# Kernel optimization log

Hardware: AMD Instinct MI355X
Metric: run time of the kernel (lower is better)

## Reference

```python
import jax, jax.numpy as jnp
import numpy as np

MEM_DIM = 2048
BATCH = 4096


def setup_inputs() -> dict:
    key = jax.random.key(0)
    ks = jax.random.split(key, 8)
    D = MEM_DIM
    scale = 1.0 / np.sqrt(D)  # torch nn.Linear default init range ~ U(-1/sqrt(D), 1/sqrt(D))
    lc = jax.random.normal(ks[0], (BATCH, D), dtype=jnp.float32)
    lh = jax.random.normal(ks[1], (BATCH, D), dtype=jnp.float32)
    rc = jax.random.normal(ks[2], (BATCH, D), dtype=jnp.float32)
    rh = jax.random.normal(ks[3], (BATCH, D), dtype=jnp.float32)
    # Fused params: columns [0:D]=input gate, [D:2D]=left forget, [2D:3D]=right forget, [3D:4D]=update
    Wl = jax.random.uniform(ks[4], (D, 4 * D), dtype=jnp.float32, minval=-scale, maxval=scale)
    Wr = jax.random.uniform(ks[5], (D, 4 * D), dtype=jnp.float32, minval=-scale, maxval=scale)
    bl = jax.random.uniform(ks[6], (4 * D,), dtype=jnp.float32, minval=-scale, maxval=scale)
    br = jax.random.uniform(ks[7], (4 * D,), dtype=jnp.float32, minval=-scale, maxval=scale)
    return {"lc": lc, "lh": lh, "rc": rc, "rh": rh, "Wl": Wl, "bl": bl, "Wr": Wr, "br": br}


def reference(lc, lh, rc, rh, Wl, bl, Wr, br):
    D = lh.shape[-1]
    # Two fused GEMMs replace 8 separate mem_dim x mem_dim linears (same math).
    g = jnp.dot(lh, Wl) + bl + jnp.dot(rh, Wr) + br  # [B, 4D]
    i = jax.nn.sigmoid(g[:, 0 * D:1 * D])   # input gate
    lf = jax.nn.sigmoid(g[:, 1 * D:2 * D])  # left forget gate
    rf = jax.nn.sigmoid(g[:, 2 * D:3 * D])  # right forget gate
    u = jnp.tanh(g[:, 3 * D:4 * D])         # cell update
    c = i * u + lf * lc + rf * rc
    h = jnp.tanh(c)
    return (c, h)
```

## Files before the change

kernel.cpp:

```cpp
#include <hip/hip_runtime.h>
#include <stdint.h>

#define D_MEM 2048
#define BATCH 4096
#define K_DIM 4096
#define N_DIM 8192

typedef __bf16 bf16x8 __attribute__((ext_vector_type(8)));
typedef float f32x4 __attribute__((ext_vector_type(4)));

typedef const void __attribute__((address_space(1)))* gas_t;
typedef void __attribute__((address_space(3)))* las_t;

__device__ __forceinline__ ushort f2b(float f) {
  union { float f; uint32_t u; } v; v.f = f;
  uint32_t u = v.u + 0x7fffu + ((v.u >> 16) & 1u);
  return (ushort)(u >> 16);
}
__device__ __forceinline__ float b2f(ushort s) {
  union { uint32_t u; float f; } v; v.u = ((uint32_t)s) << 16;
  return v.f;
}
__device__ __forceinline__ float sigm(float x) {
  return 1.0f / (1.0f + __expf(-x));
}

__global__ void cast_concat_kernel(const float* __restrict__ lh,
                                   const float* __restrict__ rh,
                                   ushort* __restrict__ A) {
  int i4 = blockIdx.x * 256 + threadIdx.x;
  int row = i4 >> 10;
  int col = (i4 & 1023) * 4;
  const float* src = (col < D_MEM) ? (lh + (size_t)row * D_MEM + col)
                                   : (rh + (size_t)row * D_MEM + (col - D_MEM));
  float4 v = *(const float4*)src;
  ushort4 o; o.x = f2b(v.x); o.y = f2b(v.y); o.z = f2b(v.z); o.w = f2b(v.w);
  *(ushort4*)(A + (size_t)row * K_DIM + col) = o;
}

__global__ void transpose_cast_kernel(const float* __restrict__ Wl,
                                      const float* __restrict__ Wr,
                                      ushort* __restrict__ Bt) {
  __shared__ float t[64 * 65];
  const float* W = blockIdx.z ? Wr : Wl;
  int n0 = blockIdx.x * 64;
  int k0 = blockIdx.y * 64;
  int tid = threadIdx.x;
#pragma unroll
  for (int i = 0; i < 4; ++i) {
    int idx = i * 256 + tid;
    int rr = idx >> 4;
    int c4 = (idx & 15) * 4;
    float4 v = *(const float4*)(W + (size_t)(k0 + rr) * N_DIM + n0 + c4);
    t[rr * 65 + c4 + 0] = v.x;
    t[rr * 65 + c4 + 1] = v.y;
    t[rr * 65 + c4 + 2] = v.z;
    t[rr * 65 + c4 + 3] = v.w;
  }
  __syncthreads();
  int kbase = (blockIdx.z ? D_MEM : 0) + k0;
#pragma unroll
  for (int i = 0; i < 4; ++i) {
    int idx = i * 256 + tid;
    int rr = idx >> 4;
    int c4 = (idx & 15) * 4;
    ushort4 o;
    o.x = f2b(t[(c4 + 0) * 65 + rr]);
    o.y = f2b(t[(c4 + 1) * 65 + rr]);
    o.z = f2b(t[(c4 + 2) * 65 + rr]);
    o.w = f2b(t[(c4 + 3) * 65 + rr]);
    *(ushort4*)(Bt + (size_t)(n0 + rr) * K_DIM + kbase + c4) = o;
  }
}

__global__ __launch_bounds__(256) void gemm_bf16_kernel(
    const ushort* __restrict__ A,
    const ushort* __restrict__ B,
    ushort* __restrict__ C) {
  const int N = N_DIM, K = K_DIM;
  __shared__ ushort As[128 * 64];
  __shared__ ushort Bs[128 * 64];
  int tid = threadIdx.x;
  int lane = tid & 63;
  int wave = tid >> 6;
  int wm = wave >> 1, wn = wave & 1;
  int q = lane >> 4, r = lane & 15;
  int m0 = blockIdx.y * 128, n0 = blockIdx.x * 128;

  int c_chunk = (tid & 7) ^ ((tid >> 3) & 7);
  int srow = tid >> 3;
  const ushort* pA = A + (size_t)(m0 + srow) * K + c_chunk * 8;
  const ushort* pB = B + (size_t)(n0 + srow) * K + c_chunk * 8;

  int aoff[4], boff[4];
#pragma unroll
  for (int f = 0; f < 4; ++f) {
    int ml = wm * 64 + f * 16 + r;
    aoff[f] = (ml * 8 + (q ^ (ml & 7))) * 16;
    int nl = wn * 64 + f * 16 + r;
    boff[f] = (nl * 8 + (q ^ (nl & 7))) * 16;
  }

  f32x4 acc[4][4];
#pragma unroll
  for (int i = 0; i < 4; ++i)
#pragma unroll
    for (int j = 0; j < 4; ++j) acc[i][j] = f32x4{0.f, 0.f, 0.f, 0.f};

  char* AsB = (char*)As;
  char* BsB = (char*)Bs;
  int ldsbase = wave * 1024;

  for (int kt = 0; kt < K / 64; ++kt) {
#pragma unroll
    for (int t2 = 0; t2 < 4; ++t2)
      __builtin_amdgcn_global_load_lds((gas_t)(pA + (size_t)t2 * 32 * K),
                                       (las_t)(AsB + t2 * 4096 + ldsbase),
                                       16, 0, 0);
#pragma unroll
    for (int t2 = 0; t2 < 4; ++t2)
      __builtin_amdgcn_global_load_lds((gas_t)(pB + (size_t)t2 * 32 * K),
                                       (las_t)(BsB + t2 * 4096 + ldsbase),
                                       16, 0, 0);
    __syncthreads();
#pragma unroll
    for (int ks = 0; ks < 2; ++ks) {
      bf16x8 af[4], bg[4];
#pragma unroll
      for (int f = 0; f < 4; ++f) {
        af[f] = *(const bf16x8*)(AsB + (aoff[f] ^ (ks * 64)));
        bg[f] = *(const bf16x8*)(BsB + (boff[f] ^ (ks * 64)));
      }
#pragma unroll
      for (int i = 0; i < 4; ++i)
#pragma unroll
        for (int j = 0; j < 4; ++j)
          acc[i][j] = __builtin_amdgcn_mfma_f32_16x16x32_bf16(
              af[i], bg[j], acc[i][j], 0, 0, 0);
    }
    __syncthreads();
    pA += 64;
    pB += 64;
  }

#pragma unroll
  for (int i = 0; i < 4; ++i) {
    int gm_base = m0 + wm * 64 + i * 16 + q * 4;
#pragma unroll
    for (int j = 0; j < 4; ++j) {
      int gn = n0 + wn * 64 + j * 16 + r;
      size_t base = (size_t)gm_base * N + gn;
#pragma unroll
      for (int e = 0; e < 4; ++e)
        C[base + (size_t)e * N] = f2b(acc[i][j][e]);
    }
  }
}

__global__ void gate_kernel(const ushort* __restrict__ G,
                            const float* __restrict__ bl,
                            const float* __restrict__ br,
                            const float* __restrict__ lc,
                            const float* __restrict__ rc,
                            float* __restrict__ out) {
  int i4 = blockIdx.x * 256 + threadIdx.x;
  int row = i4 >> 9;
  int col = (i4 & 511) * 4;
  size_t gbase = (size_t)row * N_DIM + col;

  ushort4 ui = *(const ushort4*)(G + gbase);
  ushort4 uf = *(const ushort4*)(G + gbase + 1 * D_MEM);
  ushort4 ug = *(const ushort4*)(G + gbase + 2 * D_MEM);
  ushort4 uu = *(const ushort4*)(G + gbase + 3 * D_MEM);

  float4 bli = *(const float4*)(bl + col);
  float4 blf = *(const float4*)(bl + col + 1 * D_MEM);
  float4 blr = *(const float4*)(bl + col + 2 * D_MEM);
  float4 blu = *(const float4*)(bl + col + 3 * D_MEM);
  float4 bri = *(const float4*)(br + col);
  float4 brf = *(const float4*)(br + col + 1 * D_MEM);
  float4 brr = *(const float4*)(br + col + 2 * D_MEM);
  float4 bru = *(const float4*)(br + col + 3 * D_MEM);

  float4 vlc = *(const float4*)(lc + (size_t)row * D_MEM + col);
  float4 vrc = *(const float4*)(rc + (size_t)row * D_MEM + col);

  float4 vc, vh;
  {
    float gi = b2f(ui.x) + bli.x + bri.x;
    float gf = b2f(uf.x) + blf.x + brf.x;
    float gr = b2f(ug.x) + blr.x + brr.x;
    float gu = b2f(uu.x) + blu.x + bru.x;
    vc.x = sigm(gi) * tanhf(gu) + sigm(gf) * vlc.x + sigm(gr) * vrc.x;
    vh.x = tanhf(vc.x);
  }
  {
    float gi = b2f(ui.y) + bli.y + bri.y;
    float gf = b2f(uf.y) + blf.y + brf.y;
    float gr = b2f(ug.y) + blr.y + brr.y;
    float gu = b2f(uu.y) + blu.y + bru.y;
    vc.y = sigm(gi) * tanhf(gu) + sigm(gf) * vlc.y + sigm(gr) * vrc.y;
    vh.y = tanhf(vc.y);
  }
  {
    float gi = b2f(ui.z) + bli.z + bri.z;
    float gf = b2f(uf.z) + blf.z + brf.z;
    float gr = b2f(ug.z) + blr.z + brr.z;
    float gu = b2f(uu.z) + blu.z + bru.z;
    vc.z = sigm(gi) * tanhf(gu) + sigm(gf) * vlc.z + sigm(gr) * vrc.z;
    vh.z = tanhf(vc.z);
  }
  {
    float gi = b2f(ui.w) + bli.w + bri.w;
    float gf = b2f(uf.w) + blf.w + brf.w;
    float gr = b2f(ug.w) + blr.w + brr.w;
    float gu = b2f(uu.w) + blu.w + bru.w;
    vc.w = sigm(gi) * tanhf(gu) + sigm(gf) * vlc.w + sigm(gr) * vrc.w;
    vh.w = tanhf(vc.w);
  }

  size_t obase = (size_t)row * D_MEM + col;
  *(float4*)(out + obase) = vc;
  *(float4*)(out + (size_t)BATCH * D_MEM + obase) = vh;
}

extern "C" void kernel_launch(void* const* d_in, const int* in_sizes, int n_in,
                              void* d_out, int out_size, void* d_ws, size_t ws_size,
                              hipStream_t stream) {
  const float* lc = (const float*)d_in[0];
  const float* lh = (const float*)d_in[1];
  const float* rc = (const float*)d_in[2];
  const float* rh = (const float*)d_in[3];
  const float* Wl = (const float*)d_in[4];
  const float* bl = (const float*)d_in[5];
  const float* Wr = (const float*)d_in[6];
  const float* br = (const float*)d_in[7];
  float* out = (float*)d_out;

  char* ws = (char*)d_ws;
  ushort* A  = (ushort*)ws;
  ushort* Bt = (ushort*)(ws + (size_t)32 * 1024 * 1024);
  ushort* G  = (ushort*)(ws + (size_t)96 * 1024 * 1024);

  cast_concat_kernel<<<16384, 256, 0, stream>>>(lh, rh, A);
  dim3 tg(128, 32, 2);
  transpose_cast_kernel<<<tg, 256, 0, stream>>>(Wl, Wr, Bt);
  dim3 gg(64, 32);
  gemm_bf16_kernel<<<gg, 256, 0, stream>>>(A, Bt, G);
  gate_kernel<<<8192, 256, 0, stream>>>(G, bl, br, lc, rc, out);
}
```

Baseline: 553.3 us.

## Fuse gate epilogue into GEMM by permuting weight columns per tile

The transposed weight columns are permuted so that each 128-column GEMM tile holds all four gates for the same 32 hidden units. Each lane then has the i/f/r/u accumulators for one output element and can apply the LSTM gate math directly in the GEMM epilogue. This removes the bf16 intermediate G, its write and re-read, and the separate gate kernel launch. tanhf is also replaced with an exp-based fast tanh. The epilogue now uses scalar, strided lc/rc loads and output stores instead of float4 accesses, and it adds some accuracy risk from the approximate tanh.

```diff
diff --git a/kernel.cpp b/kernel.cpp
--- a/kernel.cpp
+++ b/kernel.cpp
@@ -17,12 +17,13 @@
   uint32_t u = v.u + 0x7fffu + ((v.u >> 16) & 1u);
   return (ushort)(u >> 16);
 }
-__device__ __forceinline__ float b2f(ushort s) {
-  union { uint32_t u; float f; } v; v.u = ((uint32_t)s) << 16;
-  return v.f;
-}
 __device__ __forceinline__ float sigm(float x) {
   return 1.0f / (1.0f + __expf(-x));
+}
+__device__ __forceinline__ float fast_tanh(float x) {
+  float xx = fminf(fmaxf(x, -15.f), 15.f);
+  float t = __expf(-2.f * xx);
+  return (1.f - t) / (1.f + t);
 }
 
 __global__ void cast_concat_kernel(const float* __restrict__ lh,
@@ -59,25 +60,33 @@
   }
   __syncthreads();
   int kbase = (blockIdx.z ? D_MEM : 0) + k0;
+  int g  = n0 >> 11;
+  int jb = n0 & 2047;
 #pragma unroll
   for (int i = 0; i < 4; ++i) {
     int idx = i * 256 + tid;
     int rr = idx >> 4;
     int c4 = (idx & 15) * 4;
+    int j = jb + rr;
+    int np = ((j >> 5) << 7) + (((j >> 4) & 1) << 6) + (g << 4) + (j & 15);
     ushort4 o;
     o.x = f2b(t[(c4 + 0) * 65 + rr]);
     o.y = f2b(t[(c4 + 1) * 65 + rr]);
     o.z = f2b(t[(c4 + 2) * 65 + rr]);
     o.w = f2b(t[(c4 + 3) * 65 + rr]);
-    *(ushort4*)(Bt + (size_t)(n0 + rr) * K_DIM + kbase + c4) = o;
-  }
-}
-
-__global__ __launch_bounds__(256) void gemm_bf16_kernel(
+    *(ushort4*)(Bt + (size_t)np * K_DIM + kbase + c4) = o;
+  }
+}
+
+__global__ __launch_bounds__(256) void gemm_gate_kernel(
     const ushort* __restrict__ A,
     const ushort* __restrict__ B,
-    ushort* __restrict__ C) {
-  const int N = N_DIM, K = K_DIM;
+    const float* __restrict__ bl,
+    const float* __restrict__ br,
+    const float* __restrict__ lc,
+    const float* __restrict__ rc,
+    float* __restrict__ out) {
+  const int K = K_DIM;
   __shared__ ushort As[128 * 64];
   __shared__ ushort Bs[128 * 64];
   int tid = threadIdx.x;
@@ -143,85 +152,28 @@
     pB += 64;
   }
 
+  int colb = (blockIdx.x << 5) + (wn << 4) + r;
+  float bsum0 = bl[0 * D_MEM + colb] + br[0 * D_MEM + colb];
+  float bsum1 = bl[1 * D_MEM + colb] + br[1 * D_MEM + colb];
+  float bsum2 = bl[2 * D_MEM + colb] + br[2 * D_MEM + colb];
+  float bsum3 = bl[3 * D_MEM + colb] + br[3 * D_MEM + colb];
+  float* outc = out;
+  float* outh = out + (size_t)BATCH * D_MEM;
 #pragma unroll
   for (int i = 0; i < 4; ++i) {
-    int gm_base = m0 + wm * 64 + i * 16 + q * 4;
-#pragma unroll
-    for (int j = 0; j < 4; ++j) {
-      int gn = n0 + wn * 64 + j * 16 + r;
-      size_t base = (size_t)gm_base * N + gn;
-#pragma unroll
-      for (int e = 0; e < 4; ++e)
-        C[base + (size_t)e * N] = f2b(acc[i][j][e]);
+    int mb = m0 + wm * 64 + i * 16 + q * 4;
+#pragma unroll
+    for (int e = 0; e < 4; ++e) {
+      size_t off = (size_t)(mb + e) * D_MEM + colb;
+      float gi = acc[i][0][e] + bsum0;
+      float gf = acc[i][1][e] + bsum1;
+      float gr = acc[i][2][e] + bsum2;
+      float gu = acc[i][3][e] + bsum3;
+      float cc = sigm(gi) * fast_tanh(gu) + sigm(gf) * lc[off] + sigm(gr) * rc[off];
+      outc[off] = cc;
+      outh[off] = fast_tanh(cc);
     }
   }
-}
-
-__global__ void gate_kernel(const ushort* __restrict__ G,
-                            const float* __restrict__ bl,
-                            const float* __restrict__ br,
-                            const float* __restrict__ lc,
-                            const float* __restrict__ rc,
-                            float* __restrict__ out) {
-  int i4 = blockIdx.x * 256 + threadIdx.x;
-  int row = i4 >> 9;
-  int col = (i4 & 511) * 4;
-  size_t gbase = (size_t)row * N_DIM + col;
-
-  ushort4 ui = *(const ushort4*)(G + gbase);
-  ushort4 uf = *(const ushort4*)(G + gbase + 1 * D_MEM);
-  ushort4 ug = *(const ushort4*)(G + gbase + 2 * D_MEM);
-  ushort4 uu = *(const ushort4*)(G + gbase + 3 * D_MEM);
-
-  float4 bli = *(const float4*)(bl + col);
-  float4 blf = *(const float4*)(bl + col + 1 * D_MEM);
-  float4 blr = *(const float4*)(bl + col + 2 * D_MEM);
-  float4 blu = *(const float4*)(bl + col + 3 * D_MEM);
-  float4 bri = *(const float4*)(br + col);
-  float4 brf = *(const float4*)(br + col + 1 * D_MEM);
-  float4 brr = *(const float4*)(br + col + 2 * D_MEM);
-  float4 bru = *(const float4*)(br + col + 3 * D_MEM);
-
-  float4 vlc = *(const float4*)(lc + (size_t)row * D_MEM + col);
-  float4 vrc = *(const float4*)(rc + (size_t)row * D_MEM + col);
-
-  float4 vc, vh;
-  {
-    float gi = b2f(ui.x) + bli.x + bri.x;
-    float gf = b2f(uf.x) + blf.x + brf.x;
-    float gr = b2f(ug.x) + blr.x + brr.x;
-    float gu = b2f(uu.x) + blu.x + bru.x;
-    vc.x = sigm(gi) * tanhf(gu) + sigm(gf) * vlc.x + sigm(gr) * vrc.x;
-    vh.x = tanhf(vc.x);
-  }
-  {
-    float gi = b2f(ui.y) + bli.y + bri.y;
-    float gf = b2f(uf.y) + blf.y + brf.y;
-    float gr = b2f(ug.y) + blr.y + brr.y;
-    float gu = b2f(uu.y) + blu.y + bru.y;
-    vc.y = sigm(gi) * tanhf(gu) + sigm(gf) * vlc.y + sigm(gr) * vrc.y;
-    vh.y = tanhf(vc.y);
-  }
-  {
-    float gi = b2f(ui.z) + bli.z + bri.z;
-    float gf = b2f(uf.z) + blf.z + brf.z;
-    float gr = b2f(ug.z) + blr.z + brr.z;
-    float gu = b2f(uu.z) + blu.z + bru.z;
-    vc.z = sigm(gi) * tanhf(gu) + sigm(gf) * vlc.z + sigm(gr) * vrc.z;
-    vh.z = tanhf(vc.z);
-  }
-  {
-    float gi = b2f(ui.w) + bli.w + bri.w;
-    float gf = b2f(uf.w) + blf.w + brf.w;
-    float gr = b2f(ug.w) + blr.w + brr.w;
-    float gu = b2f(uu.w) + blu.w + bru.w;
-    vc.w = sigm(gi) * tanhf(gu) + sigm(gf) * vlc.w + sigm(gr) * vrc.w;
-    vh.w = tanhf(vc.w);
-  }
-
-  size_t obase = (size_t)row * D_MEM + col;
-  *(float4*)(out + obase) = vc;
-  *(float4*)(out + (size_t)BATCH * D_MEM + obase) = vh;
 }
 
 extern "C" void kernel_launch(void* const* d_in, const int* in_sizes, int n_in,
@@ -240,12 +192,10 @@
   char* ws = (char*)d_ws;
   ushort* A  = (ushort*)ws;
   ushort* Bt = (ushort*)(ws + (size_t)32 * 1024 * 1024);
-  ushort* G  = (ushort*)(ws + (size_t)96 * 1024 * 1024);
 
   cast_concat_kernel<<<16384, 256, 0, stream>>>(lh, rh, A);
   dim3 tg(128, 32, 2);
   transpose_cast_kernel<<<tg, 256, 0, stream>>>(Wl, Wr, Bt);
   dim3 gg(64, 32);
-  gemm_bf16_kernel<<<gg, 256, 0, stream>>>(A, Bt, G);
-  gate_kernel<<<8192, 256, 0, stream>>>(G, bl, br, lc, rc, out);
-}
+  gemm_gate_kernel<<<gg, 256, 0, stream>>>(A, Bt, bl, br, lc, rc, out);
+}
```

After: 600.4 us. 1.09x slower.
